# Kernel tuning notes

Measured on AMD Instinct MI355X. Metric: run time of the kernel, lower is better.

## Reference

```python
import jax, jax.numpy as jnp
import numpy as np

FEATURE_SIZES = (5, 5, 3, 8, 6, 2)  # sums to 29
K = 64  # truncation rank (k < min(H, W) -> truncation branch of evaluateSSVD)
B, H, W = 256, 128, 128
A = 128  # action dim (rows of weightsO)


def _conv1d(x, w, b, stride, pad):
    # x: [N, 1, L]; w: [kw]; b: scalar. Degenerate Conv3d(1,1,(1,1,kw)) along last axis.
    y = jax.lax.conv_general_dilated(x, w.reshape(1, 1, -1), (stride,), [(pad, pad)])
    return y + b


def setup_inputs() -> dict:
    key = jax.random.key(0)
    ks = jax.random.split(key, 8)
    obs = jax.random.uniform(ks[0], (B, H, W, 29), dtype=jnp.float32)
    weights1 = jax.random.normal(ks[1], (4, K, K), dtype=jnp.float32) * 0.1
    weights2 = jax.random.normal(ks[2], (4, K, K), dtype=jnp.float32) * 0.1
    weightsO = jax.random.normal(ks[3], (A, H * W), dtype=jnp.float32) * 0.02
    conv1_w = jax.random.normal(ks[4], (4,), dtype=jnp.float32) * 0.5
    conv1_b = jnp.zeros((1,), dtype=jnp.float32)
    conv2_w = jax.random.normal(ks[5], (2,), dtype=jnp.float32) * 0.5
    conv2_b = jnp.zeros((1,), dtype=jnp.float32)
    return {"obs": obs, "weights1": weights1, "weights2": weights2,
            "weightsO": weightsO, "conv1_w": conv1_w, "conv1_b": conv1_b,
            "conv2_w": conv2_w, "conv2_b": conv2_b}


def reference(obs, weights1, weights2, weightsO, conv1_w, conv1_b, conv2_w, conv2_b):
    b, h, w, d = obs.shape
    # --- feature compression: weighted sum of each plane group with arange weights ---
    feats = []
    p = 0
    for size in FEATURE_SIZES:
        wts = jnp.arange(size, dtype=obs.dtype)
        feats.append(jnp.einsum('bhwd,d->bhw', obs[..., p:p + size], wts))
        p += size
    x = jnp.stack(feats, axis=-1)  # [B,H,W,6]
    # --- conv chain along feature axis: 6 -> 4 -> 3 -> 2 -> 1 ---
    x = x.reshape(b * h * w, 1, len(FEATURE_SIZES))
    for _ in range(3):
        x = _conv1d(x, conv1_w, conv1_b[0], stride=2, pad=2)
    x = _conv1d(x, conv2_w, conv2_b[0], stride=1, pad=0)  # [B*H*W,1,1]
    M = x.reshape(b, h, w)  # per-sample matrix fed to SVD

    def eval_one(m):
        # truncated SVD (k < min(H,W) -> truncation branch of original)
        U, S, Vh = jnp.linalg.svd(m, full_matrices=False)
        Sigma = jnp.diag(S[:K])            # [k,k]
        U = U[:, :K]                       # [H,k]
        Vh = Vh[:K, :]                     # [k,W]
        U_st, _ = jnp.linalg.qr(U)         # [H,k]
        Vq, _ = jnp.linalg.qr(Vh.T)        # [W,k]
        Vh_st = Vq.T                       # [k,W]
        r = jax.nn.relu(U_st @ weights1[0])
        for i in range(1, weights1.shape[0]):
            r = jax.nn.relu(r @ weights1[i])
        r = jax.nn.relu(r @ Sigma)
        # NOTE: original loop starts at 1, so weights2[0] is intentionally unused
        for i in range(1, weights2.shape[0]):
            r = jax.nn.relu(r @ weights2[i])
        return weightsO @ (r @ Vh_st).reshape(-1)  # [A]

    return jax.vmap(eval_one)(M)  # [B, A]
```

## Files before the change

### kernel.cpp

```cpp
#include <hip/hip_runtime.h>


#define NSTR 132
#define U32_OFF 0
#define V32_OFF 8448
#define RA_OFF  16896
#define RB_OFF  25344
#define WF_OFF  33792
#define POOL_BYTES 151552

#define WAVE_FENCE() do { __asm__ __volatile__("" ::: "memory"); \
                          __builtin_amdgcn_wave_barrier();        \
                          __asm__ __volatile__("" ::: "memory"); } while (0)

template<int CTRL>
__device__ __forceinline__ double dpp_d(double x) {
    union { double d; int i[2]; } u, r;
    u.d = x;
    r.i[0] = __builtin_amdgcn_update_dpp(0, u.i[0], CTRL, 0xF, 0xF, true);
    r.i[1] = __builtin_amdgcn_update_dpp(0, u.i[1], CTRL, 0xF, 0xF, true);
    return r.d;
}
__device__ __forceinline__ double slot8_sum(double g) {
    g += dpp_d<0xB1>(g);
    g += dpp_d<0x4E>(g);
    g += dpp_d<0x141>(g);
    return g;
}

#define ROT_ANGLE(d_, g_, cc_, ss_) do {                                  \
    float d32 = (float)(d_), g32 = (float)(g_);                           \
    float h32 = sqrtf(fmaf(d32, d32, 4.0f*g32*g32));                      \
    float den = d32 + copysignf(h32, d32);                                \
    float t32 = __fdividef(2.0f*g32, den);                                \
    float c32 = rsqrtf(fmaf(t32, t32, 1.0f));                             \
    cc_ = (double)c32; ss_ = (double)(t32*c32);                           \
    double corr_ = 0.5*(3.0 - fma(cc_,cc_, ss_*ss_));                     \
    cc_ *= corr_; ss_ *= corr_;                                           \
} while (0)

__global__ __launch_bounds__(256) void k_feat(const float* __restrict__ obs,
        const float* __restrict__ c1w, const float* __restrict__ c1b,
        const float* __restrict__ c2w, const float* __restrict__ c2b,
        double* __restrict__ M)
{
    __shared__ __align__(16) float lds[256*29];
    const int t = threadIdx.x;
    const float4* obs4 = (const float4*)obs;
    float4* lds4 = (float4*)lds;
    const size_t base4 = (size_t)blockIdx.x * 1856;
    for (int idx = t; idx < 1856; idx += 256) lds4[idx] = obs4[base4 + idx];
    __syncthreads();
    const float* o = &lds[t*29];
    double f0=0,f1=0,f2=0,f3=0,f4=0,f5=0;
    #pragma unroll
    for (int d=1; d<5; ++d) f0 += (double)o[d]*d;
    #pragma unroll
    for (int d=1; d<5; ++d) f1 += (double)o[5+d]*d;
    f2 = (double)o[11] + 2.0*(double)o[12];
    #pragma unroll
    for (int d=1; d<8; ++d) f3 += (double)o[13+d]*d;
    #pragma unroll
    for (int d=1; d<6; ++d) f4 += (double)o[21+d]*d;
    f5 = (double)o[28];
    const double w0=c1w[0], w1=c1w[1], w2=c1w[2], w3=c1w[3], b1=c1b[0];
    const double cw0=c2w[0], cw1=c2w[1], b2=c2b[0];
    double y0 = b1 + f0*w2 + f1*w3;
    double y1 = b1 + f0*w0 + f1*w1 + f2*w2 + f3*w3;
    double y2 = b1 + f2*w0 + f3*w1 + f4*w2 + f5*w3;
    double y3 = b1 + f4*w0 + f5*w1;
    double z0 = b1 + y0*w2 + y1*w3;
    double z1 = b1 + y0*w0 + y1*w1 + y2*w2 + y3*w3;
    double z2 = b1 + y2*w0 + y3*w1;
    double u0 = b1 + z0*w2 + z1*w3;
    double u1 = b1 + z0*w0 + z1*w1 + z2*w2;
    double m  = b2 + u0*cw0 + u1*cw1;
    M[(size_t)blockIdx.x*256 + t] = m;
}

__global__ __launch_bounds__(512, 2) void k_svd(
        const float* __restrict__ w1g, const float* __restrict__ w2g,
        double* __restrict__ wsM)
{
    __shared__ __align__(16) char smem[POOL_BYTES];
    double* Ad = (double*)smem;
    float*  Af = (float*)smem;
    __shared__ double colnorm[128];
    __shared__ double sig_d[128];
    __shared__ double sigs_d[64];
    __shared__ float  sigf[64];
    __shared__ double tau2[2][64];
    __shared__ double vjs2[2][64];
    __shared__ int    perm[128];
    __shared__ int    redflag[8];
    __shared__ int    convflag;

    const int t = threadIdx.x;
    const int b = blockIdx.x;
    double* Mg = wsM + (size_t)b*16384;

    const int wv   = t >> 6;
    const int lk   = t & 63;
    const int slot = lk >> 3;
    const int sub  = lk & 7;

    for (int idx = t; idx < 16384; idx += 512) {
        int r = idx >> 7, c = idx & 127;
        Ad[c*NSTR + r] = Mg[idx];
    }
    __syncthreads();

    {
        const int gs = t >> 3;
        #pragma unroll
        for (int h = 0; h < 2; ++h) {
            const int c = gs + 64*h;
            const double2* P = (const double2*)&Ad[c*NSTR + 2*sub];
            double sacc = 0.0;
            #pragma unroll
            for (int m = 0; m < 8; ++m) {
                double2 v = P[m*8];
                sacc = fma(v.x, v.x, sacc); sacc = fma(v.y, v.y, sacc);
            }
            sacc = slot8_sum(sacc);
            if (sub == 0) colnorm[c] = sacc;
        }
    }
    __syncthreads();

    if (t < 128) {
        double my = colnorm[t]; int rk = 0;
        for (int c2 = 0; c2 < 128; ++c2) {
            double v = colnorm[c2];
            rk += (v > my) || (v == my && c2 < t);
        }
        perm[rk] = t;
    }
    __syncthreads();
    {
        double tmp[32]; double cn = 0.0;
        #pragma unroll
        for (int i = 0; i < 32; ++i) {
            int idx = t + i*512; int k = idx >> 7, r = idx & 127;
            tmp[i] = Ad[perm[k]*NSTR + r];
        }
        if (t < 128) cn = colnorm[perm[t]];
        __syncthreads();
        #pragma unroll
        for (int i = 0; i < 32; ++i) {
            int idx = t + i*512; int k = idx >> 7, r = idx & 127;
            Ad[k*NSTR + r] = tmp[i];
        }
        if (t < 128) colnorm[t] = cn;
    }
    __syncthreads();

    for (int sweep = 0; sweep < 16; ++sweep) {
        int big = 0;

        {
            const int ca = 16*wv + slot, cb = ca + 8;
            double2* PA = (double2*)&Ad[ca*NSTR + 2*sub];
            double2* PB = (double2*)&Ad[cb*NSTR + 2*sub];
            double2 a8[8], b8[8];
            #pragma unroll
            for (int m = 0; m < 8; ++m) { a8[m] = PA[m*8]; b8[m] = PB[m*8]; }
            double nA = colnorm[ca], nB = colnorm[cb];
            for (int s = 1; s < 8; ++s) {
                const int pa = 16*wv + (slot ^ s), pb = pa + 8;
                const int d8 = s << 3;
                const double2* QA = (const double2*)&Ad[pa*NSTR + 2*sub];
                const double2* QB = (const double2*)&Ad[pb*NSTR + 2*sub];
                double2 ya[8], yb[8];
                #pragma unroll
                for (int m = 0; m < 8; ++m) { ya[m] = QA[m*8]; yb[m] = QB[m*8]; }
                double nya = (s == 1) ? dpp_d<0x128>(nA) : __shfl_xor(nA, d8);
                double nyb = (s == 1) ? dpp_d<0x128>(nB) : __shfl_xor(nB, d8);
                double gA0=0.0, gA1=0.0, gB0=0.0, gB1=0.0;
                #pragma unroll
                for (int m = 0; m < 4; ++m) {
                    gA0 = fma(a8[m].x, ya[m].x, gA0); gA0 = fma(a8[m].y, ya[m].y, gA0);
                    gB0 = fma(b8[m].x, yb[m].x, gB0); gB0 = fma(b8[m].y, yb[m].y, gB0);
                }
                #pragma unroll
                for (int m = 4; m < 8; ++m) {
                    gA1 = fma(a8[m].x, ya[m].x, gA1); gA1 = fma(a8[m].y, ya[m].y, gA1);
                    gB1 = fma(b8[m].x, yb[m].x, gB1); gB1 = fma(b8[m].y, yb[m].y, gB1);
                }
                double gA = slot8_sum(gA0 + gA1);
                double gB = slot8_sum(gB0 + gB1);
                const int pside = (slot < (slot ^ s));
                {
                    double al = pside ? nA : nya, be = pside ? nya : nA;
                    double g2 = gA*gA, pr = al*be;
                    const bool rot = (g2 > pr*1e-20);
                    big |= rot;
                    if (__any(rot)) {
                        double cc, ss; ROT_ANGLE(be - al, gA, cc, ss);
                        cc = rot ? cc : 1.0; ss = rot ? ss : 0.0;
                        double sgn = pside ? -ss : ss;
                        #pragma unroll
                        for (int m = 0; m < 8; ++m) {
                            a8[m].x = fma(sgn, ya[m].x, cc*a8[m].x);
                            a8[m].y = fma(sgn, ya[m].y, cc*a8[m].y);
                        }
                        double cs2 = 2.0*cc*ss*gA;
                        nA = pside ? fma(cc*cc, nA, fma(ss*ss, nya, -cs2))
                                   : fma(ss*ss, nya, fma(cc*cc, nA,  cs2));
                        #pragma unroll
                        for (int m = 0; m < 8; ++m) PA[m*8] = a8[m];
                    }
                }
                {
                    double al = pside ? nB : nyb, be = pside ? nyb : nB;
                    double g2 = gB*gB, pr = al*be;
                    const bool rot = (g2 > pr*1e-20);
                    big |= rot;
                    if (__any(rot)) {
                        double cc, ss; ROT_ANGLE(be - al, gB, cc, ss);
                        cc = rot ? cc : 1.0; ss = rot ? ss : 0.0;
                        double sgn = pside ? -ss : ss;
                        #pragma unroll
                        for (int m = 0; m < 8; ++m) {
                            b8[m].x = fma(sgn, yb[m].x, cc*b8[m].x);
                            b8[m].y = fma(sgn, yb[m].y, cc*b8[m].y);
                        }
                        double cs2 = 2.0*cc*ss*gB;
                        nB = pside ? fma(cc*cc, nB, fma(ss*ss, nyb, -cs2))
                                   : fma(ss*ss, nyb, fma(cc*cc, nB,  cs2));
                        #pragma unroll
                        for (int m = 0; m < 8; ++m) PB[m*8] = b8[m];
                    }
                }
                WAVE_FENCE();
            }
            if (sub == 0) { colnorm[ca] = nA; colnorm[cb] = nB; }
        }
        __syncthreads();

        for (int r = 0; r < 15; ++r) {
            int GI, GJ;
            if (wv == 0) { GI = 15; GJ = r; }
            else { GI = (r + wv) % 15; GJ = (r - wv + 15) % 15; }
            const int pc = GI*8 + slot, qc0 = GJ*8 + slot;
            double2* Pp = (double2*)&Ad[pc*NSTR + 2*sub];
            double2* Pq = (double2*)&Ad[qc0*NSTR + 2*sub];
            double2 p8[8], q8[8];
            #pragma unroll
            for (int m = 0; m < 8; ++m) { p8[m] = Pp[m*8]; q8[m] = Pq[m*8]; }
            double np = colnorm[pc], nq = colnorm[qc0];
            bool wrote = false;
            #pragma unroll
            for (int s = 0; s < 8; ++s) {
                double g0 = 0.0, g1 = 0.0;
                #pragma unroll
                for (int m = 0; m < 4; ++m) {
                    g0 = fma(p8[m].x, q8[m].x, g0);
                    g0 = fma(p8[m].y, q8[m].y, g0);
                }
                #pragma unroll
                for (int m = 4; m < 8; ++m) {
                    g1 = fma(p8[m].x, q8[m].x, g1);
                    g1 = fma(p8[m].y, q8[m].y, g1);
                }
                double ga = slot8_sum(g0 + g1);
                double g2 = ga*ga, pr = np*nq;
                const bool rot = (g2 > pr*1e-20);
                big |= rot;
                if (__any(rot)) {
                    double cc, ss; ROT_ANGLE(nq - np, ga, cc, ss);
                    cc = rot ? cc : 1.0; ss = rot ? ss : 0.0;
                    #pragma unroll
                    for (int m = 0; m < 8; ++m) {
                        double ox = p8[m].x, oy = p8[m].y;
                        p8[m].x = fma(-ss, q8[m].x, cc*ox);
                        p8[m].y = fma(-ss, q8[m].y, cc*oy);
                        q8[m].x = fma( ss, ox, cc*q8[m].x);
                        q8[m].y = fma( ss, oy, cc*q8[m].y);
                    }
                    double cs2 = 2.0*cc*ss*ga;
                    double npn = fma(cc*cc, np, fma(ss*ss, nq, -cs2));
                    nq         = fma(ss*ss, np, fma(cc*cc, nq,  cs2));
                    np = npn;
                    wrote = true;
                }
                if (s < 7) {
                    const int d8 = ((s ^ (s+1)) << 3);
                    if (d8 == 8) {
                        #pragma unroll
                        for (int m = 0; m < 8; ++m) {
                            q8[m].x = dpp_d<0x128>(q8[m].x);
                            q8[m].y = dpp_d<0x128>(q8[m].y);
                        }
                        nq = dpp_d<0x128>(nq);
                    } else {
                        #pragma unroll
                        for (int m = 0; m < 8; ++m) {
                            q8[m].x = __shfl_xor(q8[m].x, d8);
                            q8[m].y = __shfl_xor(q8[m].y, d8);
                        }
                        nq = __shfl_xor(nq, d8);
                    }
                }
            }
            if (wrote) {
                #pragma unroll
                for (int m = 0; m < 8; ++m) Pp[m*8] = p8[m];
                const int qcf = GJ*8 + (slot ^ 7);
                double2* Pqw = (double2*)&Ad[qcf*NSTR + 2*sub];
                #pragma unroll
                for (int m = 0; m < 8; ++m) Pqw[m*8] = q8[m];
                if (sub == 0) { colnorm[pc] = np; colnorm[qcf] = nq; }
            }
            __syncthreads();
        }

        unsigned long long bb = __ballot(big);
        if (lk == 0) redflag[wv] = (bb != 0ULL) ? 1 : 0;
        __syncthreads();
        if (t == 0) {
            int any = 0;
            for (int i = 0; i < 8; ++i) any |= redflag[i];
            convflag = !any;
        }
        __syncthreads();
        if (convflag) break;
    }
    __syncthreads();

    if (t < 128) {
        double s = 0.0;
        for (int r = 0; r < 128; ++r) { double v = Ad[t*NSTR + r]; s = fma(v, v, s); }
        sig_d[t] = sqrt(s);
    }
    __syncthreads();
    if (t < 128) {
        double my = sig_d[t]; int rk = 0;
        for (int c = 0; c < 128; ++c) {
            double v = sig_d[c];
            rk += (v > my) || (v == my && c < t);
        }
        perm[rk] = t;
    }
    __syncthreads();
    if (t < 64) { sigs_d[t] = sig_d[perm[t]]; sigf[t] = (float)sig_d[perm[t]]; }
    __syncthreads();

    {
        double tmp[16];
        #pragma unroll
        for (int i = 0; i < 16; ++i) {
            int idx = t + i*512; int k = idx >> 7, r = idx & 127;
            tmp[i] = Ad[perm[k]*NSTR + r] / sigs_d[k];
        }
        __syncthreads();
        #pragma unroll
        for (int i = 0; i < 16; ++i) {
            int idx = t + i*512; int k = idx >> 7, r = idx & 127;
            Ad[k*NSTR + r] = tmp[i];
        }
    }
    __syncthreads();

    {
        const int j = t & 127, kh = (t >> 7)*16;
        double acc[16];
        #pragma unroll
        for (int m = 0; m < 16; ++m) acc[m] = 0.0;
        for (int r = 0; r < 128; ++r) {
            double mv = Mg[r*128 + j];
            #pragma unroll
            for (int m = 0; m < 16; ++m) acc[m] = fma(mv, Ad[(kh+m)*NSTR + r], acc[m]);
        }
        #pragma unroll
        for (int m = 0; m < 16; ++m) Ad[(64+kh+m)*NSTR + j] = acc[m] / sigs_d[kh+m];
    }
    __syncthreads();

    {
        const int h  = t >> 8;
        const int t5 = t & 255;
        const int CB = h * 64;
        const int g4 = t5 >> 2, s4 = t5 & 3;
        for (int j = 0; j < 64; ++j) {
            if (t5 < 64) {
                double ps = 0.0;
                for (int r = j + t5; r < 128; r += 64) { double v = Ad[(CB+j)*NSTR + r]; ps = fma(v, v, ps); }
                ps += dpp_d<0xB1>(ps);
                ps += dpp_d<0x4E>(ps);
                ps += dpp_d<0x141>(ps);
                ps += dpp_d<0x128>(ps);
                ps += __shfl_xor(ps, 16);
                ps += __shfl_xor(ps, 32);
                if (t5 == 0) {
                    double piv = Ad[(CB+j)*NSTR + j];
                    double nx = sqrt(ps);
                    double vj = piv + ((piv >= 0.0) ? nx : -nx);
                    double vn2 = ps - piv*piv + vj*vj;
                    tau2[h][j] = 2.0 / vn2;
                    vjs2[h][j] = vj;
                    Ad[(CB+j)*NSTR + j] = vj;
                }
            }
            __syncthreads();
            {
                int c = j + 1 + g4;
                if (c < 64) {
                    double w = 0.0;
                    for (int r = j + s4; r < 128; r += 4)
                        w = fma(Ad[(CB+j)*NSTR + r], Ad[(CB+c)*NSTR + r], w);
                    w += dpp_d<0xB1>(w);
                    w += dpp_d<0x4E>(w);
                    w *= tau2[h][j];
                    for (int r = j + s4; r < 128; r += 4)
                        Ad[(CB+c)*NSTR + r] -= w * Ad[(CB+j)*NSTR + r];
                }
            }
            __syncthreads();
        }
        for (int j = 63; j >= 0; --j) {
            {
                int c = j + 1 + g4;
                if (c < 64) {
                    double w = 0.0;
                    for (int r = j + s4; r < 128; r += 4)
                        w = fma(Ad[(CB+j)*NSTR + r], Ad[(CB+c)*NSTR + r], w);
                    w += dpp_d<0xB1>(w);
                    w += dpp_d<0x4E>(w);
                    w *= tau2[h][j];
                    for (int r = j + s4; r < 128; r += 4)
                        Ad[(CB+c)*NSTR + r] -= w * Ad[(CB+j)*NSTR + r];
                }
            }
            __syncthreads();
            if (t5 < 128) {
                double qv;
                if (t5 < j) qv = 0.0;
                else {
                    double vt = Ad[(CB+j)*NSTR + t5];
                    qv = ((t5 == j) ? 1.0 : 0.0) - tau2[h][j]*vjs2[h][j]*vt;
                }
                Ad[(CB+j)*NSTR + t5] = qv;
            }
            __syncthreads();
        }
    }

    {
        float tmpf[16];
        #pragma unroll
        for (int i = 0; i < 16; ++i) {
            int idx = t + i*512; int k = idx >> 7, r = idx & 127;
            tmpf[i] = (float)Ad[k*NSTR + r];
        }
        __syncthreads();
        #pragma unroll
        for (int i = 0; i < 16; ++i) {
            int idx = t + i*512; int k = idx >> 7, r = idx & 127;
            Af[U32_OFF + k*132 + r] = tmpf[i];
        }
        __syncthreads();
        #pragma unroll
        for (int i = 0; i < 16; ++i) {
            int idx = t + i*512; int k = idx >> 7, r = idx & 127;
            tmpf[i] = (float)Ad[(64+k)*NSTR + r];
        }
        __syncthreads();
        #pragma unroll
        for (int i = 0; i < 16; ++i) {
            int idx = t + i*512; int k = idx >> 7, r = idx & 127;
            Af[V32_OFF + k*132 + r] = tmpf[i];
        }
    }
    __syncthreads();

    int SRCO = U32_OFF, DSTO = RA_OFF;
    const int n = t & 63, ib = (t >> 6)*16;
    for (int layer = 0; layer < 7; ++layer) {
        const float* wptr = (layer < 4) ? (w1g + layer*4096) : (w2g + (layer-3)*4096);
        for (int idx = t; idx < 4096; idx += 512) Af[WF_OFF + idx] = wptr[idx];
        __syncthreads();
        float acc[16];
        #pragma unroll
        for (int m = 0; m < 16; ++m) acc[m] = 0.f;
        for (int kk = 0; kk < 64; ++kk) {
            float wv2 = Af[WF_OFF + kk*64 + n];
            const float4* s4v = (const float4*)&Af[SRCO + kk*132 + ib];
            #pragma unroll
            for (int q4 = 0; q4 < 4; ++q4) {
                float4 v4 = s4v[q4];
                acc[q4*4+0] = fmaf(v4.x, wv2, acc[q4*4+0]);
                acc[q4*4+1] = fmaf(v4.y, wv2, acc[q4*4+1]);
                acc[q4*4+2] = fmaf(v4.z, wv2, acc[q4*4+2]);
                acc[q4*4+3] = fmaf(v4.w, wv2, acc[q4*4+3]);
            }
        }
        float sc = (layer == 3) ? sigf[n] : 1.f;
        #pragma unroll
        for (int q4 = 0; q4 < 4; ++q4) {
            float4 o;
            o.x = fmaxf(acc[q4*4+0], 0.f)*sc;
            o.y = fmaxf(acc[q4*4+1], 0.f)*sc;
            o.z = fmaxf(acc[q4*4+2], 0.f)*sc;
            o.w = fmaxf(acc[q4*4+3], 0.f)*sc;
            ((float4*)&Af[DSTO + n*132 + ib])[q4] = o;
        }
        __syncthreads();
        SRCO = DSTO; DSTO = (DSTO == RA_OFF) ? RB_OFF : RA_OFF;
    }

    {
        float* Tb = (float*)((char*)wsM + (size_t)b*131072);
        const int j2 = t & 127, ih = (t >> 7)*32;
        float acc2[32];
        #pragma unroll
        for (int m = 0; m < 32; ++m) acc2[m] = 0.f;
        for (int kk = 0; kk < 64; ++kk) {
            float vv = Af[V32_OFF + kk*132 + j2];
            const float4* r4 = (const float4*)&Af[RA_OFF + kk*132 + ih];
            #pragma unroll
            for (int q4 = 0; q4 < 8; ++q4) {
                float4 v4 = r4[q4];
                acc2[q4*4+0] = fmaf(v4.x, vv, acc2[q4*4+0]);
                acc2[q4*4+1] = fmaf(v4.y, vv, acc2[q4*4+1]);
                acc2[q4*4+2] = fmaf(v4.z, vv, acc2[q4*4+2]);
                acc2[q4*4+3] = fmaf(v4.w, vv, acc2[q4*4+3]);
            }
        }
        #pragma unroll
        for (int m = 0; m < 32; ++m) Tb[(size_t)(ih+m)*128 + j2] = acc2[m];
    }
}

__global__ __launch_bounds__(256) void k_out(const char* __restrict__ wsbase,
        const float* __restrict__ wO, float* __restrict__ part)
{
    __shared__ float Wt[128*65];
    __shared__ float Tt[8*64];
    const int t = threadIdx.x;
    const int bt = blockIdx.x & 31, ks = blockIdx.x >> 5;
    const int a = t & 127, bh = (t >> 7)*4;
    float acc[4] = {0.f, 0.f, 0.f, 0.f};
    for (int cc = 0; cc < 32; ++cc) {
        const int kbase = ks*2048 + cc*64;
        __syncthreads();
        for (int idx = t; idx < 8192; idx += 256) {
            int aa = idx >> 6, nn = idx & 63;
            Wt[aa*65 + nn] = wO[aa*16384 + kbase + nn];
        }
        for (int idx = t; idx < 512; idx += 256) {
            int bl = idx >> 6, nn = idx & 63;
            const float* Tb = (const float*)(wsbase + (size_t)(bt*8 + bl)*131072);
            Tt[bl*64 + nn] = Tb[kbase + nn];
        }
        __syncthreads();
        for (int nn = 0; nn < 64; ++nn) {
            float wv = Wt[a*65 + nn];
            #pragma unroll
            for (int m = 0; m < 4; ++m) acc[m] = fmaf(Tt[(bh+m)*64 + nn], wv, acc[m]);
        }
    }
    #pragma unroll
    for (int m = 0; m < 4; ++m)
        part[ks*32768 + (bt*8 + bh + m)*128 + a] = acc[m];
}

__global__ __launch_bounds__(256) void k_red(const float* __restrict__ part,
                                             float* __restrict__ out)
{
    int i = blockIdx.x*256 + threadIdx.x;
    float s = 0.f;
    #pragma unroll
    for (int ks = 0; ks < 8; ++ks) s += part[ks*32768 + i];
    out[i] = s;
}

extern "C" void kernel_launch(void* const* d_in, const int* in_sizes, int n_in,
                              void* d_out, int out_size, void* d_ws, size_t ws_size,
                              hipStream_t stream)
{
    (void)in_sizes; (void)n_in; (void)out_size; (void)ws_size;
    const float* obs = (const float*)d_in[0];
    const float* w1  = (const float*)d_in[1];
    const float* w2  = (const float*)d_in[2];
    const float* wO  = (const float*)d_in[3];
    const float* c1w = (const float*)d_in[4];
    const float* c1b = (const float*)d_in[5];
    const float* c2w = (const float*)d_in[6];
    const float* c2b = (const float*)d_in[7];
    double* M = (double*)d_ws;
    float* part = (float*)((char*)d_ws + 33554432);

    k_feat<<<dim3(16384), dim3(256), 0, stream>>>(obs, c1w, c1b, c2w, c2b, M);
    k_svd <<<dim3(256),   dim3(512), 0, stream>>>(w1, w2, M);
    k_out <<<dim3(256),   dim3(256), 0, stream>>>((const char*)d_ws, wO, part);
    k_red <<<dim3(128),   dim3(256), 0, stream>>>(part, (float*)d_out);
}
```

Before: 1.923 ms.

## Use fast scaled Givens rotations with per-column scale factors in Jacobi SVD

Replaces the standard one-sided Jacobi rotations with fast-Givens style updates. Each column keeps a scale factor d and its inverse, so the column update needs one FMA per element instead of a multiply plus an FMA. The true Gram entry is recovered by multiplying with the scale products. Scales are folded back into the matrix every four sweeps and once after convergence to avoid under/overflow. This adds extra shuffles, shared-memory state and periodic renormalisation passes, and may change numerical accuracy.

```diff
diff --git a/kernel.cpp b/kernel.cpp
--- a/kernel.cpp
+++ b/kernel.cpp
@@ -28,15 +28,17 @@
     return g;
 }
 
-#define ROT_ANGLE(d_, g_, cc_, ss_) do {                                  \
+#define ROT_FG(d_, g_, tt_, cc_, se_, rc_) do {                           \
     float d32 = (float)(d_), g32 = (float)(g_);                           \
     float h32 = sqrtf(fmaf(d32, d32, 4.0f*g32*g32));                      \
     float den = d32 + copysignf(h32, d32);                                \
     float t32 = __fdividef(2.0f*g32, den);                                \
-    float c32 = rsqrtf(fmaf(t32, t32, 1.0f));                             \
-    cc_ = (double)c32; ss_ = (double)(t32*c32);                           \
-    double corr_ = 0.5*(3.0 - fma(cc_,cc_, ss_*ss_));                     \
-    cc_ *= corr_; ss_ *= corr_;                                           \
+    tt_ = (double)t32;                                                    \
+    double opt2_ = fma(tt_, tt_, 1.0);                                    \
+    double c0_ = (double)rsqrtf(fmaf(t32, t32, 1.0f));                    \
+    cc_ = c0_*0.5*(3.0 - c0_*c0_*opt2_);                                 \
+    rc_ = cc_*opt2_;                                                      \
+    se_ = cc_*tt_;                                                        \
 } while (0)
 
 __global__ __launch_bounds__(256) void k_feat(const float* __restrict__ obs,
@@ -86,6 +88,8 @@
     double* Ad = (double*)smem;
     float*  Af = (float*)smem;
     __shared__ double colnorm[128];
+    __shared__ double dcol[128];
+    __shared__ double invdcol[128];
     __shared__ double sig_d[128];
     __shared__ double sigs_d[64];
     __shared__ float  sigf[64];
@@ -151,11 +155,20 @@
             int idx = t + i*512; int k = idx >> 7, r = idx & 127;
             Ad[k*NSTR + r] = tmp[i];
         }
-        if (t < 128) colnorm[t] = cn;
+        if (t < 128) { colnorm[t] = cn; dcol[t] = 1.0; invdcol[t] = 1.0; }
     }
     __syncthreads();
 
     for (int sweep = 0; sweep < 16; ++sweep) {
+        if (sweep && (sweep & 3) == 0) {
+            for (int idx = t; idx < 16384; idx += 512) {
+                int r = idx >> 7, c = idx & 127;
+                Ad[c*NSTR + r] *= dcol[c];
+            }
+            __syncthreads();
+            if (t < 128) { dcol[t] = 1.0; invdcol[t] = 1.0; }
+            __syncthreads();
+        }
         int big = 0;
 
         {
@@ -166,6 +179,8 @@
             #pragma unroll
             for (int m = 0; m < 8; ++m) { a8[m] = PA[m*8]; b8[m] = PB[m*8]; }
             double nA = colnorm[ca], nB = colnorm[cb];
+            double dA = dcol[ca], iA = invdcol[ca];
+            double dB = dcol[cb], iB = invdcol[cb];
             for (int s = 1; s < 8; ++s) {
                 const int pa = 16*wv + (slot ^ s), pb = pa + 8;
                 const int d8 = s << 3;
@@ -174,8 +189,14 @@
                 double2 ya[8], yb[8];
                 #pragma unroll
                 for (int m = 0; m < 8; ++m) { ya[m] = QA[m*8]; yb[m] = QB[m*8]; }
-                double nya = (s == 1) ? dpp_d<0x128>(nA) : __shfl_xor(nA, d8);
-                double nyb = (s == 1) ? dpp_d<0x128>(nB) : __shfl_xor(nB, d8);
+                double nya, dya, iya, nyb, dyb, iyb;
+                if (s == 1) {
+                    nya = dpp_d<0x128>(nA); dya = dpp_d<0x128>(dA); iya = dpp_d<0x128>(iA);
+                    nyb = dpp_d<0x128>(nB); dyb = dpp_d<0x128>(dB); iyb = dpp_d<0x128>(iB);
+                } else {
+                    nya = __shfl_xor(nA, d8); dya = __shfl_xor(dA, d8); iya = __shfl_xor(iA, d8);
+                    nyb = __shfl_xor(nB, d8); dyb = __shfl_xor(dB, d8); iyb = __shfl_xor(iB, d8);
+                }
                 double gA0=0.0, gA1=0.0, gB0=0.0, gB1=0.0;
                 #pragma unroll
                 for (int m = 0; m < 4; ++m) {
@@ -187,8 +208,8 @@
                     gA1 = fma(a8[m].x, ya[m].x, gA1); gA1 = fma(a8[m].y, ya[m].y, gA1);
                     gB1 = fma(b8[m].x, yb[m].x, gB1); gB1 = fma(b8[m].y, yb[m].y, gB1);
                 }
-                double gA = slot8_sum(gA0 + gA1);
-                double gB = slot8_sum(gB0 + gB1);
+                double gA = slot8_sum(gA0 + gA1) * (dA*dya);
+                double gB = slot8_sum(gB0 + gB1) * (dB*dyb);
                 const int pside = (slot < (slot ^ s));
                 {
                     double al = pside ? nA : nya, be = pside ? nya : nA;
@@ -196,17 +217,20 @@
                     const bool rot = (g2 > pr*1e-20);
                     big |= rot;
                     if (__any(rot)) {
-                        double cc, ss; ROT_ANGLE(be - al, gA, cc, ss);
-                        cc = rot ? cc : 1.0; ss = rot ? ss : 0.0;
-                        double sgn = pside ? -ss : ss;
+                        double tt, cc, se, rc; ROT_FG(be - al, gA, tt, cc, se, rc);
+                        tt = rot ? tt : 0.0; cc = rot ? cc : 1.0;
+                        se = rot ? se : 0.0; rc = rot ? rc : 1.0;
+                        double coef = tt * dya * iA;
+                        double sgn = pside ? -coef : coef;
                         #pragma unroll
                         for (int m = 0; m < 8; ++m) {
-                            a8[m].x = fma(sgn, ya[m].x, cc*a8[m].x);
-                            a8[m].y = fma(sgn, ya[m].y, cc*a8[m].y);
+                            a8[m].x = fma(sgn, ya[m].x, a8[m].x);
+                            a8[m].y = fma(sgn, ya[m].y, a8[m].y);
                         }
-                        double cs2 = 2.0*cc*ss*gA;
-                        nA = pside ? fma(cc*cc, nA, fma(ss*ss, nya, -cs2))
-                                   : fma(ss*ss, nya, fma(cc*cc, nA,  cs2));
+                        double cs2 = 2.0*cc*se*gA;
+                        nA = pside ? fma(cc*cc, nA, fma(se*se, nya, -cs2))
+                                   : fma(se*se, nya, fma(cc*cc, nA,  cs2));
+                        dA *= cc; iA *= rc;
                         #pragma unroll
                         for (int m = 0; m < 8; ++m) PA[m*8] = a8[m];
                     }
@@ -217,24 +241,31 @@
                     const bool rot = (g2 > pr*1e-20);
                     big |= rot;
                     if (__any(rot)) {
-                        double cc, ss; ROT_ANGLE(be - al, gB, cc, ss);
-                        cc = rot ? cc : 1.0; ss = rot ? ss : 0.0;
-                        double sgn = pside ? -ss : ss;
+                        double tt, cc, se, rc; ROT_FG(be - al, gB, tt, cc, se, rc);
+                        tt = rot ? tt : 0.0; cc = rot ? cc : 1.0;
+                        se = rot ? se : 0.0; rc = rot ? rc : 1.0;
+                        double coef = tt * dyb * iB;
+                        double sgn = pside ? -coef : coef;
                         #pragma unroll
                         for (int m = 0; m < 8; ++m) {
-                            b8[m].x = fma(sgn, yb[m].x, cc*b8[m].x);
-                            b8[m].y = fma(sgn, yb[m].y, cc*b8[m].y);
+                            b8[m].x = fma(sgn, yb[m].x, b8[m].x);
+                            b8[m].y = fma(sgn, yb[m].y, b8[m].y);
                         }
-                        double cs2 = 2.0*cc*ss*gB;
-                        nB = pside ? fma(cc*cc, nB, fma(ss*ss, nyb, -cs2))
-                                   : fma(ss*ss, nyb, fma(cc*cc, nB,  cs2));
+                        double cs2 = 2.0*cc*se*gB;
+                        nB = pside ? fma(cc*cc, nB, fma(se*se, nyb, -cs2))
+                                   : fma(se*se, nyb, fma(cc*cc, nB,  cs2));
+                        dB *= cc; iB *= rc;
                         #pragma unroll
                         for (int m = 0; m < 8; ++m) PB[m*8] = b8[m];
                     }
                 }
                 WAVE_FENCE();
             }
-            if (sub == 0) { colnorm[ca] = nA; colnorm[cb] = nB; }
+            if (sub == 0) {
+                colnorm[ca] = nA; colnorm[cb] = nB;
+                dcol[ca] = dA; dcol[cb] = dB;
+                invdcol[ca] = iA; invdcol[cb] = iB;
+            }
         }
         __syncthreads();
 
@@ -249,6 +280,8 @@
             #pragma unroll
             for (int m = 0; m < 8; ++m) { p8[m] = Pp[m*8]; q8[m] = Pq[m*8]; }
             double np = colnorm[pc], nq = colnorm[qc0];
+            double dp = dcol[pc], ip = invdcol[pc];
+            double dq = dcol[qc0], iq = invdcol[qc0];
             bool wrote = false;
             #pragma unroll
             for (int s = 0; s < 8; ++s) {
@@ -263,25 +296,29 @@
                     g1 = fma(p8[m].x, q8[m].x, g1);
                     g1 = fma(p8[m].y, q8[m].y, g1);
                 }
-                double ga = slot8_sum(g0 + g1);
+                double ga = slot8_sum(g0 + g1) * (dp*dq);
                 double g2 = ga*ga, pr = np*nq;
                 const bool rot = (g2 > pr*1e-20);
                 big |= rot;
                 if (__any(rot)) {
-                    double cc, ss; ROT_ANGLE(nq - np, ga, cc, ss);
-                    cc = rot ? cc : 1.0; ss = rot ? ss : 0.0;
+                    double tt, cc, se, rc; ROT_FG(nq - np, ga, tt, cc, se, rc);
+                    tt = rot ? tt : 0.0; cc = rot ? cc : 1.0;
+                    se = rot ? se : 0.0; rc = rot ? rc : 1.0;
+                    double arp = tt * dq * ip;
+                    double brq = tt * dp * iq;
                     #pragma unroll
                     for (int m = 0; m < 8; ++m) {
                         double ox = p8[m].x, oy = p8[m].y;
-                        p8[m].x = fma(-ss, q8[m].x, cc*ox);
-                        p8[m].y = fma(-ss, q8[m].y, cc*oy);
-                        q8[m].x = fma( ss, ox, cc*q8[m].x);
-                        q8[m].y = fma( ss, oy, cc*q8[m].y);
+                        p8[m].x = fma(-arp, q8[m].x, ox);
+                        p8[m].y = fma(-arp, q8[m].y, oy);
+                        q8[m].x = fma( brq, ox, q8[m].x);
+                        q8[m].y = fma( brq, oy, q8[m].y);
                     }
-                    double cs2 = 2.0*cc*ss*ga;
-                    double npn = fma(cc*cc, np, fma(ss*ss, nq, -cs2));
-                    nq         = fma(ss*ss, np, fma(cc*cc, nq,  cs2));
+                    double cs2 = 2.0*cc*se*ga;
+                    double npn = fma(cc*cc, np, fma(se*se, nq, -cs2));
+                    nq         = fma(se*se, np, fma(cc*cc, nq,  cs2));
                     np = npn;
+                    dp *= cc; ip *= rc; dq *= cc; iq *= rc;
                     wrote = true;
                 }
                 if (s < 7) {
@@ -292,14 +329,14 @@
                             q8[m].x = dpp_d<0x128>(q8[m].x);
                             q8[m].y = dpp_d<0x128>(q8[m].y);
                         }
-                        nq = dpp_d<0x128>(nq);
+                        nq = dpp_d<0x128>(nq); dq = dpp_d<0x128>(dq); iq = dpp_d<0x128>(iq);
                     } else {
                         #pragma unroll
                         for (int m = 0; m < 8; ++m) {
                             q8[m].x = __shfl_xor(q8[m].x, d8);
                             q8[m].y = __shfl_xor(q8[m].y, d8);
                         }
-                        nq = __shfl_xor(nq, d8);
+                        nq = __shfl_xor(nq, d8); dq = __shfl_xor(dq, d8); iq = __shfl_xor(iq, d8);
                     }
                 }
             }
@@ -310,7 +347,11 @@
                 double2* Pqw = (double2*)&Ad[qcf*NSTR + 2*sub];
                 #pragma unroll
                 for (int m = 0; m < 8; ++m) Pqw[m*8] = q8[m];
-                if (sub == 0) { colnorm[pc] = np; colnorm[qcf] = nq; }
+                if (sub == 0) {
+                    colnorm[pc] = np; colnorm[qcf] = nq;
+                    dcol[pc] = dp; dcol[qcf] = dq;
+                    invdcol[pc] = ip; invdcol[qcf] = iq;
+                }
             }
             __syncthreads();
         }
@@ -325,6 +366,12 @@
         }
         __syncthreads();
         if (convflag) break;
+    }
+    __syncthreads();
+
+    for (int idx = t; idx < 16384; idx += 512) {
+        int r = idx >> 7, c = idx & 127;
+        Ad[c*NSTR + r] *= dcol[c];
     }
     __syncthreads();
 
```

Measured after the change: 1.957 ms. Within noise of the previous version (+1.8%).
